# Performance work log

Hardware: AMD Instinct MI355X
Metric: run time of the kernel (lower is better)

The kernel has to match this reference:

```python
import jax, jax.numpy as jnp
import numpy as np

N = 50000
E = 800000
IN_DIM = 128
HEADS = 8
OUT_DIM = 32
NEG_SLOPE = 0.2


def setup_inputs() -> dict:
    key = jax.random.key(0)
    k1, k2, k3, k4, k5 = jax.random.split(key, 5)
    x = jax.random.normal(k1, (N, IN_DIM), dtype=jnp.float32)
    edge_index = jax.random.randint(k2, (2, E), 0, N, dtype=jnp.int64)
    batch = jnp.zeros((N,), dtype=jnp.int64)
    # GATConv params: glorot-style scale
    W = jax.random.normal(k3, (IN_DIM, HEADS * OUT_DIM), dtype=jnp.float32) * (1.0 / np.sqrt(IN_DIM))
    att_src = jax.random.normal(k4, (HEADS, OUT_DIM), dtype=jnp.float32) * (1.0 / np.sqrt(OUT_DIM))
    att_dst = jax.random.normal(k5, (HEADS, OUT_DIM), dtype=jnp.float32) * (1.0 / np.sqrt(OUT_DIM))
    bias = jnp.zeros((OUT_DIM,), dtype=jnp.float32)
    return {"x": x, "edge_index": edge_index, "batch": batch,
            "W": W, "att_src": att_src, "att_dst": att_dst, "bias": bias}


def reference(x, edge_index, batch, W, att_src, att_dst, bias):
    n = x.shape[0]
    h = (x @ W).reshape(n, HEADS, OUT_DIM)            # [N, H, C]
    a_src = jnp.einsum('nhc,hc->nh', h, att_src)       # [N, H]
    a_dst = jnp.einsum('nhc,hc->nh', h, att_dst)       # [N, H]
    # add self-loops (PyG default add_self_loops=True)
    loops = jnp.arange(n, dtype=edge_index.dtype)
    src = jnp.concatenate([edge_index[0], loops])
    dst = jnp.concatenate([edge_index[1], loops])
    e = jax.nn.leaky_relu(a_src[src] + a_dst[dst], NEG_SLOPE)  # [E+N, H]
    # scatter-softmax over incoming edges of each dst node
    m = jax.ops.segment_max(e, dst, num_segments=n)    # [N, H]
    m = jax.lax.stop_gradient(m)
    ex = jnp.exp(e - m[dst])
    denom = jax.ops.segment_sum(ex, dst, num_segments=n)
    alpha = ex / denom[dst]                            # [E+N, H]
    msg = h[src] * alpha[..., None]                    # [E+N, H, C]
    out = jax.ops.segment_sum(msg, dst, num_segments=n)  # [N, H, C]
    out = out.mean(axis=1) + bias                      # concat=False -> head mean
    return out
```

## Files before the change

### kernel.cpp

```cpp
#include <hip/hip_runtime.h>

#define IN_DIM 128
#define HC 256
#define HEADS 8
#define OUT_DIM 32
#define NEG_SLOPE 0.2f

typedef unsigned short ushort_t;
typedef unsigned int uint_t;
typedef __attribute__((ext_vector_type(8))) short bf16x8;
typedef __attribute__((ext_vector_type(4))) float floatx4;

__device__ inline ushort_t f2bf(float f) {
    uint_t u = __float_as_uint(f);
    u = (u + 0x7FFF + ((u >> 16) & 1)) >> 16;
    return (ushort_t)u;
}
__device__ inline float bf2f(ushort_t u) {
    return __uint_as_float(((uint_t)u) << 16);
}

__global__ __launch_bounds__(256) void prep_w(const float* __restrict__ W,
                                              ushort_t* __restrict__ Wf) {
    int t = blockIdx.x * 256 + threadIdx.x;
    int lane = t & 63;
    int ks = (t >> 6) & 3;
    int nt = t >> 8;
    int n = nt * 16 + (lane & 15);
    int k0 = ks * 32 + (lane >> 4) * 8;
    ushort_t v[8];
#pragma unroll
    for (int j = 0; j < 8; j++) v[j] = f2bf(W[(size_t)(k0 + j) * HC + n]);
    uint4 pk;
    pk.x = v[0] | ((uint_t)v[1] << 16);
    pk.y = v[2] | ((uint_t)v[3] << 16);
    pk.z = v[4] | ((uint_t)v[5] << 16);
    pk.w = v[6] | ((uint_t)v[7] << 16);
    *(uint4*)&Wf[(size_t)t * 8] = pk;
}

__global__ __launch_bounds__(256) void gemm_mfma(const float* __restrict__ x,
                                                 const ushort_t* __restrict__ Wf,
                                                 ushort_t* __restrict__ h2, int N) {
    __shared__ ushort_t xs[128 * 136];
    const int tid = threadIdx.x;
    const int row0 = blockIdx.x * 128;
#pragma unroll
    for (int i = 0; i < 16; i++) {
        int slot = tid + i * 256;
        int r = slot >> 5, kq = slot & 31;
        int gr = row0 + r;
        float4 v = (gr < N) ? *(const float4*)&x[(size_t)gr * IN_DIM + kq * 4]
                            : make_float4(0.f, 0.f, 0.f, 0.f);
        uint2 pk;
        pk.x = f2bf(v.x) | ((uint_t)f2bf(v.y) << 16);
        pk.y = f2bf(v.z) | ((uint_t)f2bf(v.w) << 16);
        *(uint2*)&xs[r * 136 + kq * 4] = pk;
    }
    __syncthreads();

    const int lane = tid & 63;
    const int w = tid >> 6;
    const int wm = (w & 1) * 64;
    const int colblk = blockIdx.y * 128 + (w >> 1) * 64;
    const int m15 = lane & 15, quad = lane >> 4;

    floatx4 acc[4][4] = {};
#pragma unroll
    for (int ks = 0; ks < 4; ks++) {
        bf16x8 a[4], b[4];
#pragma unroll
        for (int mt = 0; mt < 4; mt++)
            a[mt] = *(const bf16x8*)&xs[(wm + mt * 16 + m15) * 136 + ks * 32 + quad * 8];
#pragma unroll
        for (int nt = 0; nt < 4; nt++) {
            int ntg = (colblk >> 4) + nt;
            b[nt] = *(const bf16x8*)&Wf[(size_t)(((ntg * 4 + ks) * 64) + lane) * 8];
        }
#pragma unroll
        for (int mt = 0; mt < 4; mt++)
#pragma unroll
            for (int nt = 0; nt < 4; nt++)
                acc[mt][nt] = __builtin_amdgcn_mfma_f32_16x16x32_bf16(a[mt], b[nt], acc[mt][nt], 0, 0, 0);
    }

    const int cbase = colblk + m15;
#pragma unroll
    for (int mt = 0; mt < 4; mt++) {
#pragma unroll
        for (int reg = 0; reg < 4; reg++) {
            int gr = row0 + wm + mt * 16 + quad * 4 + reg;
            if (gr < N) {
#pragma unroll
                for (int nt = 0; nt < 4; nt++)
                    h2[(size_t)gr * HC + cbase + nt * 16] = f2bf(acc[mt][nt][reg]);
            }
        }
    }
}

__global__ __launch_bounds__(256) void attn_coeff(const ushort_t* __restrict__ h2,
                                                  const float* __restrict__ att_src,
                                                  const float* __restrict__ att_dst,
                                                  float* __restrict__ a_src,
                                                  float* __restrict__ a_dst, int N) {
    int wave = threadIdx.x >> 6;
    int lane = threadIdx.x & 63;
    int n = blockIdx.x * 4 + wave;
    if (n >= N) return;
    ushort4 hv = *(const ushort4*)&h2[(size_t)n * HC + lane * 4];
    float4 as = *(const float4*)&att_src[lane * 4];
    float4 ad = *(const float4*)&att_dst[lane * 4];
    float hx = bf2f(hv.x), hy = bf2f(hv.y), hz = bf2f(hv.z), hw = bf2f(hv.w);
    float s = hx * as.x + hy * as.y + hz * as.z + hw * as.w;
    float d = hx * ad.x + hy * ad.y + hz * ad.z + hw * ad.w;
#pragma unroll
    for (int off = 1; off < 8; off <<= 1) {
        s += __shfl_xor(s, off, 64);
        d += __shfl_xor(d, off, 64);
    }
    if ((lane & 7) == 0) {
        int head = lane >> 3;
        a_src[n * HEADS + head] = s;
        a_dst[n * HEADS + head] = d;
    }
}

__global__ void count_deg(const int* __restrict__ dst, int* __restrict__ deg, int E) {
    int i = blockIdx.x * 256 + threadIdx.x;
    if (i < E) atomicAdd(&deg[dst[i]], 1);
}

__global__ __launch_bounds__(1024) void scan_pass1(const int* __restrict__ deg,
                                                   int* __restrict__ rs,
                                                   int* __restrict__ bsum, int N) {
    __shared__ int wsum[16], wexcl[16];
    int tid = threadIdx.x, lane = tid & 63, w = tid >> 6;
    int base = blockIdx.x * 4096 + tid * 4;
    int v[4];
#pragma unroll
    for (int j = 0; j < 4; j++) v[j] = (base + j < N) ? deg[base + j] : 0;
    int s = v[0] + v[1] + v[2] + v[3];
    int xsc = s;
#pragma unroll
    for (int off = 1; off < 64; off <<= 1) {
        int t = __shfl_up(xsc, off, 64);
        if (lane >= off) xsc += t;
    }
    if (lane == 63) wsum[w] = xsc;
    __syncthreads();
    if (w == 0 && lane < 16) {
        int y = wsum[lane], z = y;
#pragma unroll
        for (int off = 1; off < 16; off <<= 1) {
            int t = __shfl_up(z, off, 64);
            if (lane >= off) z += t;
        }
        wexcl[lane] = z - y;
        if (lane == 15) bsum[blockIdx.x] = z;
    }
    __syncthreads();
    int e = wexcl[w] + (xsc - s);
#pragma unroll
    for (int j = 0; j < 4; j++) {
        if (base + j < N) rs[base + j] = e;
        e += v[j];
    }
}

__global__ __launch_bounds__(64) void scan_pass2(int* __restrict__ bsum, int nb) {
    int lane = threadIdx.x;
    int v = (lane < nb) ? bsum[lane] : 0;
    int xsc = v;
#pragma unroll
    for (int off = 1; off < 64; off <<= 1) {
        int t = __shfl_up(xsc, off, 64);
        if (lane >= off) xsc += t;
    }
    if (lane < nb) bsum[lane] = xsc - v;
    if (lane == nb - 1) bsum[nb] = xsc;
}

__global__ void scan_pass3(int* __restrict__ rs, int* __restrict__ cursor,
                           const int* __restrict__ bsum, int N, int nb) {
    int i = blockIdx.x * 256 + threadIdx.x;
    if (i < N) {
        int v = rs[i] + bsum[i >> 12];
        rs[i] = v;
        cursor[i] = v;
    }
    if (i == 0) rs[N] = bsum[nb];
}

__global__ void scatter_edges(const int* __restrict__ src, const int* __restrict__ dst,
                              int* __restrict__ cursor, int* __restrict__ csr_src, int E) {
    int i = blockIdx.x * 256 + threadIdx.x;
    if (i < E) {
        int pos = atomicAdd(&cursor[dst[i]], 1);
        csr_src[pos] = src[i];
    }
}

__global__ __launch_bounds__(256) void aggregate(const ushort_t* __restrict__ h2,
                                                 const float* __restrict__ a_src,
                                                 const float* __restrict__ a_dst,
                                                 const int* __restrict__ row_start,
                                                 const int* __restrict__ csr_src,
                                                 const float* __restrict__ bias,
                                                 float* __restrict__ out, int N) {
    int wave = threadIdx.x >> 6;
    int lane = threadIdx.x & 63;
    int n = blockIdx.x * 4 + wave;
    if (n >= N) return;
    int head = lane >> 3;
    int coff = head * OUT_DIM + (lane & 7) * 4;

    float adst = a_dst[n * HEADS + head];
    float e = a_src[n * HEADS + head] + adst;
    e = fmaxf(e, NEG_SLOPE * e);
    float p = __expf(e);
    ushort4 hv = *(const ushort4*)&h2[(size_t)n * HC + coff];
    float ax = p * bf2f(hv.x), ay = p * bf2f(hv.y), az = p * bf2f(hv.z), aw = p * bf2f(hv.w);
    float l = p;

    int kb = row_start[n], ke = row_start[n + 1];
    int k = kb;
    for (; k + 3 < ke; k += 4) {
        int s0 = csr_src[k], s1 = csr_src[k + 1], s2 = csr_src[k + 2], s3 = csr_src[k + 3];
        float e0 = a_src[s0 * HEADS + head] + adst;
        float e1 = a_src[s1 * HEADS + head] + adst;
        float e2 = a_src[s2 * HEADS + head] + adst;
        float e3 = a_src[s3 * HEADS + head] + adst;
        ushort4 g0 = *(const ushort4*)&h2[(size_t)s0 * HC + coff];
        ushort4 g1 = *(const ushort4*)&h2[(size_t)s1 * HC + coff];
        ushort4 g2 = *(const ushort4*)&h2[(size_t)s2 * HC + coff];
        ushort4 g3 = *(const ushort4*)&h2[(size_t)s3 * HC + coff];
        e0 = fmaxf(e0, NEG_SLOPE * e0); e1 = fmaxf(e1, NEG_SLOPE * e1);
        e2 = fmaxf(e2, NEG_SLOPE * e2); e3 = fmaxf(e3, NEG_SLOPE * e3);
        float p0 = __expf(e0), p1 = __expf(e1), p2 = __expf(e2), p3 = __expf(e3);
        ax += p0 * bf2f(g0.x) + p1 * bf2f(g1.x) + p2 * bf2f(g2.x) + p3 * bf2f(g3.x);
        ay += p0 * bf2f(g0.y) + p1 * bf2f(g1.y) + p2 * bf2f(g2.y) + p3 * bf2f(g3.y);
        az += p0 * bf2f(g0.z) + p1 * bf2f(g1.z) + p2 * bf2f(g2.z) + p3 * bf2f(g3.z);
        aw += p0 * bf2f(g0.w) + p1 * bf2f(g1.w) + p2 * bf2f(g2.w) + p3 * bf2f(g3.w);
        l += p0 + p1 + p2 + p3;
    }
    for (; k < ke; k++) {
        int s0 = csr_src[k];
        float e0 = a_src[s0 * HEADS + head] + adst;
        ushort4 g0 = *(const ushort4*)&h2[(size_t)s0 * HC + coff];
        e0 = fmaxf(e0, NEG_SLOPE * e0);
        float p0 = __expf(e0);
        ax += p0 * bf2f(g0.x); ay += p0 * bf2f(g0.y);
        az += p0 * bf2f(g0.z); aw += p0 * bf2f(g0.w);
        l += p0;
    }

    float inv = 1.f / l;
    float rx = ax * inv, ry = ay * inv, rz = az * inv, rw = aw * inv;
#pragma unroll
    for (int off = 8; off < 64; off <<= 1) {
        rx += __shfl_xor(rx, off, 64);
        ry += __shfl_xor(ry, off, 64);
        rz += __shfl_xor(rz, off, 64);
        rw += __shfl_xor(rw, off, 64);
    }
    if (head == 0) {
        int c4 = (lane & 7) * 4;
        float4 b = *(const float4*)&bias[c4];
        float4 o = make_float4(0.125f * rx + b.x, 0.125f * ry + b.y,
                               0.125f * rz + b.z, 0.125f * rw + b.w);
        *(float4*)&out[(size_t)n * OUT_DIM + c4] = o;
    }
}

extern "C" void kernel_launch(void* const* d_in, const int* in_sizes, int n_in,
                              void* d_out, int out_size, void* d_ws, size_t ws_size,
                              hipStream_t stream) {
    const float* x       = (const float*)d_in[0];
    const int*   eidx    = (const int*)d_in[1];
    const float* W       = (const float*)d_in[3];
    const float* att_src = (const float*)d_in[4];
    const float* att_dst = (const float*)d_in[5];
    const float* bias    = (const float*)d_in[6];
    float* out = (float*)d_out;

    const int N = in_sizes[0] / IN_DIM;
    const int E = in_sizes[1] / 2;
    const int* esrc = eidx;
    const int* edst = eidx + E;

    char* wsb = (char*)d_ws;
    size_t off = 0;
    auto alloc = [&](size_t bytes) -> void* {
        void* p = wsb + off;
        off = (off + bytes + 255) & ~(size_t)255;
        return p;
    };
    ushort_t* h2       = (ushort_t*)alloc((size_t)N * HC * 2);
    ushort_t* Wf       = (ushort_t*)alloc((size_t)IN_DIM * HC * 2);
    float*    a_src    = (float*)alloc((size_t)N * HEADS * 4);
    float*    a_dst    = (float*)alloc((size_t)N * HEADS * 4);
    int*      deg      = (int*)alloc((size_t)N * 4);
    int*      cursor   = (int*)alloc((size_t)N * 4);
    int*      row_start= (int*)alloc((size_t)(N + 1) * 4);
    int*      csr_src  = (int*)alloc((size_t)E * 4);
    const int nb = (N + 4095) / 4096;
    int*      bsum     = (int*)alloc((size_t)(nb + 1) * 4);

    hipLaunchKernelGGL(prep_w, dim3(16), dim3(256), 0, stream, W, Wf);
    hipLaunchKernelGGL(gemm_mfma, dim3((N + 127) / 128, 2), dim3(256), 0, stream, x, Wf, h2, N);
    hipLaunchKernelGGL(attn_coeff, dim3((N + 3) / 4), dim3(256), 0, stream,
                       h2, att_src, att_dst, a_src, a_dst, N);
    hipMemsetAsync(deg, 0, (size_t)N * 4, stream);
    hipLaunchKernelGGL(count_deg, dim3((E + 255) / 256), dim3(256), 0, stream, edst, deg, E);
    hipLaunchKernelGGL(scan_pass1, dim3(nb), dim3(1024), 0, stream, deg, row_start, bsum, N);
    hipLaunchKernelGGL(scan_pass2, dim3(1), dim3(64), 0, stream, bsum, nb);
    hipLaunchKernelGGL(scan_pass3, dim3((N + 255) / 256), dim3(256), 0, stream,
                       row_start, cursor, bsum, N, nb);
    hipLaunchKernelGGL(scatter_edges, dim3((E + 255) / 256), dim3(256), 0, stream,
                       esrc, edst, cursor, csr_src, E);
    hipLaunchKernelGGL(aggregate, dim3((N + 3) / 4), dim3(256), 0, stream,
                       h2, a_src, a_dst, row_start, csr_src, bias, out, N);
}
```

Measured before the change: 260.9 us.

## Fuse attention coefficients into GEMM, merge scan passes, vectorize edge kernels

Attention source/destination coefficients are now computed in the GEMM epilogue from fp32 accumulators using cross-lane shuffles, which removes the separate attn_coeff pass that re-read h2. Scan passes 2 and 3 are merged so each block rescans the block sums itself, saving one launch. The count_deg and scatter_edges kernels now load four edges per thread through int4 reads. The aggregate kernel unrolls to eight edges and uses readfirstlane on row bounds and neighbor indices so they are held in scalar registers. The coefficients are now computed from unrounded accumulators, so they differ slightly from the previous bf16-based values, and the int4 loads assume the edge arrays are 16-byte aligned.

```diff
diff --git a/kernel.cpp b/kernel.cpp
--- a/kernel.cpp
+++ b/kernel.cpp
@@ -41,7 +41,11 @@
 
 __global__ __launch_bounds__(256) void gemm_mfma(const float* __restrict__ x,
                                                  const ushort_t* __restrict__ Wf,
-                                                 ushort_t* __restrict__ h2, int N) {
+                                                 const float* __restrict__ att_s,
+                                                 const float* __restrict__ att_d,
+                                                 ushort_t* __restrict__ h2,
+                                                 float* __restrict__ a_src,
+                                                 float* __restrict__ a_dst, int N) {
     __shared__ ushort_t xs[128 * 136];
     const int tid = threadIdx.x;
     const int row0 = blockIdx.x * 128;
@@ -85,50 +89,54 @@
     }
 
     const int cbase = colblk + m15;
+    const int head0 = colblk >> 5;
+    float as0 = att_s[colblk + m15],      as1 = att_s[colblk + 16 + m15];
+    float as2 = att_s[colblk + 32 + m15], as3 = att_s[colblk + 48 + m15];
+    float ad0 = att_d[colblk + m15],      ad1 = att_d[colblk + 16 + m15];
+    float ad2 = att_d[colblk + 32 + m15], ad3 = att_d[colblk + 48 + m15];
 #pragma unroll
     for (int mt = 0; mt < 4; mt++) {
 #pragma unroll
         for (int reg = 0; reg < 4; reg++) {
             int gr = row0 + wm + mt * 16 + quad * 4 + reg;
+            float sA = acc[mt][0][reg] * as0 + acc[mt][1][reg] * as1;
+            float sB = acc[mt][2][reg] * as2 + acc[mt][3][reg] * as3;
+            float dA = acc[mt][0][reg] * ad0 + acc[mt][1][reg] * ad1;
+            float dB = acc[mt][2][reg] * ad2 + acc[mt][3][reg] * ad3;
+#pragma unroll
+            for (int off = 1; off < 16; off <<= 1) {
+                sA += __shfl_xor(sA, off, 64);
+                sB += __shfl_xor(sB, off, 64);
+                dA += __shfl_xor(dA, off, 64);
+                dB += __shfl_xor(dB, off, 64);
+            }
             if (gr < N) {
 #pragma unroll
                 for (int nt = 0; nt < 4; nt++)
                     h2[(size_t)gr * HC + cbase + nt * 16] = f2bf(acc[mt][nt][reg]);
+                if (m15 == 0) {
+                    a_src[gr * HEADS + head0] = sA;
+                    a_src[gr * HEADS + head0 + 1] = sB;
+                    a_dst[gr * HEADS + head0] = dA;
+                    a_dst[gr * HEADS + head0 + 1] = dB;
+                }
             }
         }
-    }
-}
-
-__global__ __launch_bounds__(256) void attn_coeff(const ushort_t* __restrict__ h2,
-                                                  const float* __restrict__ att_src,
-                                                  const float* __restrict__ att_dst,
-                                                  float* __restrict__ a_src,
-                                                  float* __restrict__ a_dst, int N) {
-    int wave = threadIdx.x >> 6;
-    int lane = threadIdx.x & 63;
-    int n = blockIdx.x * 4 + wave;
-    if (n >= N) return;
-    ushort4 hv = *(const ushort4*)&h2[(size_t)n * HC + lane * 4];
-    float4 as = *(const float4*)&att_src[lane * 4];
-    float4 ad = *(const float4*)&att_dst[lane * 4];
-    float hx = bf2f(hv.x), hy = bf2f(hv.y), hz = bf2f(hv.z), hw = bf2f(hv.w);
-    float s = hx * as.x + hy * as.y + hz * as.z + hw * as.w;
-    float d = hx * ad.x + hy * ad.y + hz * ad.z + hw * ad.w;
-#pragma unroll
-    for (int off = 1; off < 8; off <<= 1) {
-        s += __shfl_xor(s, off, 64);
-        d += __shfl_xor(d, off, 64);
-    }
-    if ((lane & 7) == 0) {
-        int head = lane >> 3;
-        a_src[n * HEADS + head] = s;
-        a_dst[n * HEADS + head] = d;
     }
 }
 
 __global__ void count_deg(const int* __restrict__ dst, int* __restrict__ deg, int E) {
     int i = blockIdx.x * 256 + threadIdx.x;
-    if (i < E) atomicAdd(&deg[dst[i]], 1);
+    int base = i * 4;
+    if (base + 3 < E) {
+        int4 d = *(const int4*)&dst[base];
+        atomicAdd(&deg[d.x], 1);
+        atomicAdd(&deg[d.y], 1);
+        atomicAdd(&deg[d.z], 1);
+        atomicAdd(&deg[d.w], 1);
+    } else {
+        for (int j = base; j < E; j++) atomicAdd(&deg[dst[j]], 1);
+    }
 }
 
 __global__ __launch_bounds__(1024) void scan_pass1(const int* __restrict__ deg,
@@ -168,36 +176,49 @@
     }
 }
 
-__global__ __launch_bounds__(64) void scan_pass2(int* __restrict__ bsum, int nb) {
-    int lane = threadIdx.x;
-    int v = (lane < nb) ? bsum[lane] : 0;
-    int xsc = v;
-#pragma unroll
-    for (int off = 1; off < 64; off <<= 1) {
-        int t = __shfl_up(xsc, off, 64);
-        if (lane >= off) xsc += t;
-    }
-    if (lane < nb) bsum[lane] = xsc - v;
-    if (lane == nb - 1) bsum[nb] = xsc;
-}
-
-__global__ void scan_pass3(int* __restrict__ rs, int* __restrict__ cursor,
-                           const int* __restrict__ bsum, int N, int nb) {
-    int i = blockIdx.x * 256 + threadIdx.x;
+__global__ __launch_bounds__(256) void scan_pass23(int* __restrict__ rs,
+                                                   int* __restrict__ cursor,
+                                                   const int* __restrict__ bsum,
+                                                   int N, int nb) {
+    __shared__ int soff, stot;
+    int tid = threadIdx.x;
+    if (tid < 64) {
+        int v = (tid < nb) ? bsum[tid] : 0;
+        int incl = v;
+#pragma unroll
+        for (int off = 1; off < 64; off <<= 1) {
+            int t = __shfl_up(incl, off, 64);
+            if (tid >= off) incl += t;
+        }
+        int chunk = blockIdx.x >> 4;
+        int off_ = __shfl(incl - v, chunk, 64);
+        int tot_ = __shfl(incl, nb - 1, 64);
+        if (tid == 0) { soff = off_; stot = tot_; }
+    }
+    __syncthreads();
+    int i = blockIdx.x * 256 + tid;
     if (i < N) {
-        int v = rs[i] + bsum[i >> 12];
+        int v = rs[i] + soff;
         rs[i] = v;
         cursor[i] = v;
     }
-    if (i == 0) rs[N] = bsum[nb];
+    if (i == N) rs[N] = stot;
 }
 
 __global__ void scatter_edges(const int* __restrict__ src, const int* __restrict__ dst,
                               int* __restrict__ cursor, int* __restrict__ csr_src, int E) {
     int i = blockIdx.x * 256 + threadIdx.x;
-    if (i < E) {
-        int pos = atomicAdd(&cursor[dst[i]], 1);
-        csr_src[pos] = src[i];
+    int base = i * 4;
+    if (base + 3 < E) {
+        int4 s = *(const int4*)&src[base];
+        int4 d = *(const int4*)&dst[base];
+        csr_src[atomicAdd(&cursor[d.x], 1)] = s.x;
+        csr_src[atomicAdd(&cursor[d.y], 1)] = s.y;
+        csr_src[atomicAdd(&cursor[d.z], 1)] = s.z;
+        csr_src[atomicAdd(&cursor[d.w], 1)] = s.w;
+    } else {
+        for (int j = base; j < E; j++)
+            csr_src[atomicAdd(&cursor[dst[j]], 1)] = src[j];
     }
 }
 
@@ -214,6 +235,7 @@
     if (n >= N) return;
     int head = lane >> 3;
     int coff = head * OUT_DIM + (lane & 7) * 4;
+    int hoff = head;
 
     float adst = a_dst[n * HEADS + head];
     float e = a_src[n * HEADS + head] + adst;
@@ -223,30 +245,36 @@
     float ax = p * bf2f(hv.x), ay = p * bf2f(hv.y), az = p * bf2f(hv.z), aw = p * bf2f(hv.w);
     float l = p;
 
-    int kb = row_start[n], ke = row_start[n + 1];
+    int kb = __builtin_amdgcn_readfirstlane(row_start[n]);
+    int ke = __builtin_amdgcn_readfirstlane(row_start[n + 1]);
     int k = kb;
-    for (; k + 3 < ke; k += 4) {
-        int s0 = csr_src[k], s1 = csr_src[k + 1], s2 = csr_src[k + 2], s3 = csr_src[k + 3];
-        float e0 = a_src[s0 * HEADS + head] + adst;
-        float e1 = a_src[s1 * HEADS + head] + adst;
-        float e2 = a_src[s2 * HEADS + head] + adst;
-        float e3 = a_src[s3 * HEADS + head] + adst;
-        ushort4 g0 = *(const ushort4*)&h2[(size_t)s0 * HC + coff];
-        ushort4 g1 = *(const ushort4*)&h2[(size_t)s1 * HC + coff];
-        ushort4 g2 = *(const ushort4*)&h2[(size_t)s2 * HC + coff];
-        ushort4 g3 = *(const ushort4*)&h2[(size_t)s3 * HC + coff];
-        e0 = fmaxf(e0, NEG_SLOPE * e0); e1 = fmaxf(e1, NEG_SLOPE * e1);
-        e2 = fmaxf(e2, NEG_SLOPE * e2); e3 = fmaxf(e3, NEG_SLOPE * e3);
-        float p0 = __expf(e0), p1 = __expf(e1), p2 = __expf(e2), p3 = __expf(e3);
-        ax += p0 * bf2f(g0.x) + p1 * bf2f(g1.x) + p2 * bf2f(g2.x) + p3 * bf2f(g3.x);
-        ay += p0 * bf2f(g0.y) + p1 * bf2f(g1.y) + p2 * bf2f(g2.y) + p3 * bf2f(g3.y);
-        az += p0 * bf2f(g0.z) + p1 * bf2f(g1.z) + p2 * bf2f(g2.z) + p3 * bf2f(g3.z);
-        aw += p0 * bf2f(g0.w) + p1 * bf2f(g1.w) + p2 * bf2f(g2.w) + p3 * bf2f(g3.w);
-        l += p0 + p1 + p2 + p3;
+    for (; k + 7 < ke; k += 8) {
+        int sidx[8];
+        ushort4 g[8];
+        float ev[8];
+#pragma unroll
+        for (int j = 0; j < 8; j++)
+            sidx[j] = __builtin_amdgcn_readfirstlane(csr_src[k + j]);
+#pragma unroll
+        for (int j = 0; j < 8; j++) {
+            g[j] = *(const ushort4*)&h2[(size_t)sidx[j] * HC + coff];
+            ev[j] = a_src[sidx[j] * HEADS + hoff];
+        }
+#pragma unroll
+        for (int j = 0; j < 8; j++) {
+            float ej = ev[j] + adst;
+            ej = fmaxf(ej, NEG_SLOPE * ej);
+            float pj = __expf(ej);
+            ax += pj * bf2f(g[j].x);
+            ay += pj * bf2f(g[j].y);
+            az += pj * bf2f(g[j].z);
+            aw += pj * bf2f(g[j].w);
+            l += pj;
+        }
     }
     for (; k < ke; k++) {
-        int s0 = csr_src[k];
-        float e0 = a_src[s0 * HEADS + head] + adst;
+        int s0 = __builtin_amdgcn_readfirstlane(csr_src[k]);
+        float e0 = a_src[s0 * HEADS + hoff] + adst;
         ushort4 g0 = *(const ushort4*)&h2[(size_t)s0 * HC + coff];
         e0 = fmaxf(e0, NEG_SLOPE * e0);
         float p0 = __expf(e0);
@@ -308,16 +336,14 @@
     int*      bsum     = (int*)alloc((size_t)(nb + 1) * 4);
 
     hipLaunchKernelGGL(prep_w, dim3(16), dim3(256), 0, stream, W, Wf);
-    hipLaunchKernelGGL(gemm_mfma, dim3((N + 127) / 128, 2), dim3(256), 0, stream, x, Wf, h2, N);
-    hipLaunchKernelGGL(attn_coeff, dim3((N + 3) / 4), dim3(256), 0, stream,
-                       h2, att_src, att_dst, a_src, a_dst, N);
+    hipLaunchKernelGGL(gemm_mfma, dim3((N + 127) / 128, 2), dim3(256), 0, stream,
+                       x, Wf, att_src, att_dst, h2, a_src, a_dst, N);
     hipMemsetAsync(deg, 0, (size_t)N * 4, stream);
-    hipLaunchKernelGGL(count_deg, dim3((E + 255) / 256), dim3(256), 0, stream, edst, deg, E);
+    hipLaunchKernelGGL(count_deg, dim3((E / 4 + 255) / 256), dim3(256), 0, stream, edst, deg, E);
     hipLaunchKernelGGL(scan_pass1, dim3(nb), dim3(1024), 0, stream, deg, row_start, bsum, N);
-    hipLaunchKernelGGL(scan_pass2, dim3(1), dim3(64), 0, stream, bsum, nb);
-    hipLaunchKernelGGL(scan_pass3, dim3((N + 255) / 256), dim3(256), 0, stream,
+    hipLaunchKernelGGL(scan_pass23, dim3((N + 256) / 256), dim3(256), 0, stream,
                        row_start, cursor, bsum, N, nb);
-    hipLaunchKernelGGL(scatter_edges, dim3((E + 255) / 256), dim3(256), 0, stream,
+    hipLaunchKernelGGL(scatter_edges, dim3((E / 4 + 255) / 256), dim3(256), 0, stream,
                        esrc, edst, cursor, csr_src, E);
     hipLaunchKernelGGL(aggregate, dim3((N + 3) / 4), dim3(256), 0, stream,
                        h2, a_src, a_dst, row_start, csr_src, bias, out, N);
```

New measurement: 260.9 us. Within noise of the previous version (-0.0%).
